# Optimization experiments

Hardware: AMD Instinct MI355X
Metric: run time of the kernel (lower is better)

Reference implementation:

```python
import jax, jax.numpy as jnp
import numpy as np

B, T, D, R, DFF = 4, 4096, 1024, 128, 4096
WINDOW = 1024
EPS = 1e-6


def rmsnorm(x, w):
    x32 = x.astype(jnp.float32)
    rms = jax.lax.rsqrt(jnp.mean(x32 * x32, axis=-1, keepdims=True) + EPS)
    return (x32 * rms).astype(x.dtype) * w


def rope(x, cos, sin):
    # x: (B, T, R); cos/sin: (T, R//2)
    d = x.shape[-1] // 2
    x1, x2 = x[..., :d], x[..., d:]
    return jnp.concatenate([x1 * cos + x2 * sin, -x1 * sin + x2 * cos], axis=-1)


def setup_inputs() -> dict:
    key = jax.random.key(0)
    ks = jax.random.split(key, 12)
    s = 0.02  # realistic weight scale
    return {
        "x": jax.random.normal(ks[0], (B, T, D), jnp.float32),
        "Uq": jax.random.normal(ks[1], (R, D), jnp.float32) * s,
        "Uk": jax.random.normal(ks[2], (R, D), jnp.float32) * s,
        "Uv": jax.random.normal(ks[3], (R, D), jnp.float32) * s,
        "cos": jnp.cos(jnp.outer(jnp.arange(T, dtype=jnp.float32),
                                 1.0 / (10000.0 ** (jnp.arange(R // 2, dtype=jnp.float32) / (R // 2))))),
        "sin": jnp.sin(jnp.outer(jnp.arange(T, dtype=jnp.float32),
                                 1.0 / (10000.0 ** (jnp.arange(R // 2, dtype=jnp.float32) / (R // 2))))),
        "ln1_w": jnp.ones((D,), jnp.float32),
        "ln2_w": jnp.ones((D,), jnp.float32),
        "Wo": jax.random.normal(ks[4], (D, R), jnp.float32) * s,
        "w1": jax.random.normal(ks[5], (DFF, D), jnp.float32) * s,
        "w3": jax.random.normal(ks[6], (DFF, D), jnp.float32) * s,
        "w2": jax.random.normal(ks[7], (D, DFF), jnp.float32) * s,
        "window_size": WINDOW,
    }


def reference(x, Uq, Uk, Uv, cos, sin, ln1_w, ln2_w, Wo, w1, w3, w2, window_size):
    Bx, Tx, _ = x.shape
    rank = Uq.shape[0]
    normed = rmsnorm(x, ln1_w)
    q = rope(normed @ Uq.T, cos, sin)  # (B, T, R)
    k = rope(normed @ Uk.T, cos, sin)
    v = normed @ Uv.T
    # windowed causal single-head SDPA
    scale = 1.0 / jnp.sqrt(jnp.float32(rank))
    scores = jnp.einsum("btr,bsr->bts", q, k) * scale  # (B, T, T)
    row = jnp.arange(Tx)[:, None]
    col = jnp.arange(Tx)[None, :]
    mask = (col <= row) & ((row - col) <= window_size)
    scores = jnp.where(mask, scores, jnp.float32(-jnp.inf))
    attn = jax.nn.softmax(scores, axis=-1)
    y = jnp.einsum("bts,bsr->btr", attn, v)  # (B, T, R)
    x = x + y @ Wo.T
    h = rmsnorm(x, ln2_w)
    ffn = ((h @ w1.T) * jax.nn.silu(h @ w3.T)) @ w2.T
    return x + ffn
```

## Files before the change

### kernel.cpp

```cpp
#include <hip/hip_runtime.h>
#include <hip/hip_bf16.h>
#include <stdint.h>

#define BT   16384
#define TT   4096
#define NB   4
#define DD   1024
#define RR   128
#define DFFC 4096

typedef __bf16 bf16_8 __attribute__((ext_vector_type(8)));
typedef float  f32x4  __attribute__((ext_vector_type(4)));

__device__ __forceinline__ void async16(const void* g, void* l) {
  __builtin_amdgcn_global_load_lds((__attribute__((address_space(1))) void*)(g),
                                   (__attribute__((address_space(3))) void*)(l),
                                   16, 0, 0);
}

__global__ __launch_bounds__(256) void cvt_k(const float* __restrict__ src,
                                             __hip_bfloat16* __restrict__ dst, int n4) {
  const int i = blockIdx.x * 256 + threadIdx.x;
  if (i >= n4) return;
  const float4 v = ((const float4*)src)[i];
  __hip_bfloat16* o = dst + (size_t)i * 4;
  o[0] = __float2bfloat16(v.x);
  o[1] = __float2bfloat16(v.y);
  o[2] = __float2bfloat16(v.z);
  o[3] = __float2bfloat16(v.w);
}

__global__ __launch_bounds__(256) void rmsnorm_k(const float* __restrict__ x,
                                                 const float* __restrict__ wgt,
                                                 __hip_bfloat16* __restrict__ out) {
  const int row = blockIdx.x;
  const int t = threadIdx.x;
  const float4 v = ((const float4*)(x + (size_t)row * DD))[t];
  float ss = v.x*v.x + v.y*v.y + v.z*v.z + v.w*v.w;
  #pragma unroll
  for (int m = 1; m < 64; m <<= 1) ss += __shfl_xor(ss, m, 64);
  __shared__ float red[4];
  if ((t & 63) == 0) red[t >> 6] = ss;
  __syncthreads();
  ss = red[0] + red[1] + red[2] + red[3];
  const float rms = rsqrtf(ss * (1.0f / DD) + 1e-6f);
  const float4 wv = ((const float4*)wgt)[t];
  __hip_bfloat16* o = out + (size_t)row * DD + t * 4;
  o[0] = __float2bfloat16(v.x * rms * wv.x);
  o[1] = __float2bfloat16(v.y * rms * wv.y);
  o[2] = __float2bfloat16(v.z * rms * wv.z);
  o[3] = __float2bfloat16(v.w * rms * wv.w);
}

__global__ __launch_bounds__(256) void rope_k(const __hip_bfloat16* __restrict__ qkv,
                                              const float* __restrict__ cosb,
                                              const float* __restrict__ sinb,
                                              __hip_bfloat16* __restrict__ qr,
                                              __hip_bfloat16* __restrict__ kr) {
  const int idx = blockIdx.x * 256 + threadIdx.x;
  const int row = idx >> 6;
  const int i = idx & 63;
  const int tpos = row & (TT - 1);
  const float c = cosb[tpos * 64 + i];
  const float s = sinb[tpos * 64 + i];
  const size_t base = (size_t)row * 384;
  const float q1 = __bfloat162float(qkv[base + i]);
  const float q2 = __bfloat162float(qkv[base + 64 + i]);
  const float k1 = __bfloat162float(qkv[base + 128 + i]);
  const float k2 = __bfloat162float(qkv[base + 192 + i]);
  const size_t ob = (size_t)row * 128;
  qr[ob + i]      = __float2bfloat16( q1 * c + q2 * s);
  qr[ob + 64 + i] = __float2bfloat16(-q1 * s + q2 * c);
  kr[ob + i]      = __float2bfloat16( k1 * c + k2 * s);
  kr[ob + 64 + i] = __float2bfloat16(-k1 * s + k2 * c);
}

__global__ __launch_bounds__(256) void vtrans_k(const __hip_bfloat16* __restrict__ qkv,
                                                __hip_bfloat16* __restrict__ Vt) {
  const int b = blockIdx.y, t0 = blockIdx.x * 64, t = threadIdx.x;
  #pragma unroll
  for (int i = 0; i < 4; ++i) {
    const int flat8 = i * 256 + t;
    const int row = flat8 >> 4;
    const int d8 = (flat8 & 15) * 8;
    const bf16_8 v = *(const bf16_8*)&qkv[((size_t)(b * TT + t0 + row)) * 384 + 256 + d8];
    #pragma unroll
    for (int j = 0; j < 8; ++j)
      ((__bf16*)Vt)[((size_t)(b * 128 + d8 + j)) * TT + t0 + row] = v[j];
  }
}

enum { EPI_BF16 = 0, EPI_RESID = 1, EPI_GATE = 2 };

template <int EPI>
__global__ __launch_bounds__(256) void gemm_bt(
    const __hip_bfloat16* __restrict__ A,
    const __hip_bfloat16* __restrict__ Bw,
    const float* __restrict__ resid,
    const __hip_bfloat16* __restrict__ gate,
    __hip_bfloat16* __restrict__ outb,
    float* __restrict__ outf,
    int N, int K) {
  __shared__ __hip_bfloat16 As[128 * 64];
  __shared__ __hip_bfloat16 Bs[128 * 64];
  const int t = threadIdx.x;
  const int w = t >> 6, lane = t & 63;
  const int wm = w >> 1, wn = w & 1;
  const int quad = lane >> 4, l16 = lane & 15;
  const int m0 = blockIdx.y * 128, n0 = blockIdx.x * 128;

  const __hip_bfloat16* Ab = A + (size_t)m0 * K;
  const __hip_bfloat16* Bb = Bw + (size_t)n0 * K;

  const int rloc = w * 8 + (lane >> 3);
  const int c0 = (((lane & 7) ^ ((lane >> 3) & 7)) << 3);
  const int swz = (l16 & 7);

  f32x4 acc[4][4] = {};

  for (int k0 = 0; k0 < K; k0 += 64) {
    #pragma unroll
    for (int j = 0; j < 4; ++j) {
      async16(Ab + (size_t)(j * 32 + rloc) * K + k0 + c0, &As[j * 2048 + w * 512]);
      async16(Bb + (size_t)(j * 32 + rloc) * K + k0 + c0, &Bs[j * 2048 + w * 512]);
    }
    __syncthreads();
    #pragma unroll
    for (int kc = 0; kc < 2; ++kc) {
      bf16_8 af[4], bfr[4];
      #pragma unroll
      for (int i = 0; i < 4; ++i) {
        const int pos = (((kc * 4 + quad) ^ swz) << 3);
        af[i]  = *(const bf16_8*)&As[(wm * 64 + i * 16 + l16) * 64 + pos];
        bfr[i] = *(const bf16_8*)&Bs[(wn * 64 + i * 16 + l16) * 64 + pos];
      }
      #pragma unroll
      for (int mt = 0; mt < 4; ++mt) {
        #pragma unroll
        for (int nt = 0; nt < 4; ++nt)
          acc[mt][nt] = __builtin_amdgcn_mfma_f32_16x16x32_bf16(af[mt], bfr[nt], acc[mt][nt], 0, 0, 0);
      }
    }
    __syncthreads();
  }

  #pragma unroll
  for (int mt = 0; mt < 4; ++mt) {
    #pragma unroll
    for (int nt = 0; nt < 4; ++nt) {
      #pragma unroll
      for (int r = 0; r < 4; ++r) {
        const int row = m0 + wm * 64 + mt * 16 + quad * 4 + r;
        const int col = n0 + wn * 64 + nt * 16 + l16;
        const size_t idx = (size_t)row * N + col;
        const float v = acc[mt][nt][r];
        if (EPI == EPI_BF16) {
          outb[idx] = __float2bfloat16(v);
        } else if (EPI == EPI_RESID) {
          outf[idx] = resid[idx] + v;
        } else {
          const float sv = v / (1.0f + __expf(-v));
          outb[idx] = __float2bfloat16(__bfloat162float(gate[idx]) * sv);
        }
      }
    }
  }
}

#define G256_BAR()  asm volatile("s_barrier" ::: "memory")
#define G256_VMW(N) asm volatile("s_waitcnt vmcnt(" #N ")" ::: "memory")

#define G256_DSA(mh_) \
  { _Pragma("unroll") for (int mt = 0; mt < 4; ++mt) { \
      const int rb_ = (rbA + (mh_) * 64 + mt * 16) * 64; \
      a[mt][0] = *(const bf16_8*)&Ac[rb_ + p0]; \
      a[mt][1] = *(const bf16_8*)&Ac[rb_ + p1]; } }

#define G256_DSB(nh_) \
  { _Pragma("unroll") for (int nt = 0; nt < 2; ++nt) { \
      const int rb_ = (rbB + (nh_) * 32 + nt * 16) * 64; \
      b[nt][0] = *(const bf16_8*)&Bc[rb_ + p0]; \
      b[nt][1] = *(const bf16_8*)&Bc[rb_ + p1]; } }

#define G256_MMA(mh_, nh_) \
  { __builtin_amdgcn_s_setprio(1); \
    _Pragma("unroll") for (int kk = 0; kk < 2; ++kk) \
      _Pragma("unroll") for (int mt = 0; mt < 4; ++mt) \
        _Pragma("unroll") for (int nt = 0; nt < 2; ++nt) \
          acc[(mh_) * 4 + mt][(nh_) * 2 + nt] = __builtin_amdgcn_mfma_f32_16x16x32_bf16( \
              a[mt][kk], b[nt][kk], acc[(mh_) * 4 + mt][(nh_) * 2 + nt], 0, 0, 0); \
    __builtin_amdgcn_s_setprio(0); }

#define G256_TILE(CUR, kt_) { \
    const __hip_bfloat16* Ac = As[CUR]; \
    const __hip_bfloat16* Bc = Bs[CUR]; \
    const int nb_ = (CUR) ^ 1; \
    const bool pf = ((kt_) + 1) < NT; \
    const int kn = ((kt_) + 1) << 6; \
     \
    G256_DSA(0); G256_DSB(0); \
    if (pf) { stageA(0, nb_, kn); stageB(0, nb_, kn); } \
    G256_BAR(); G256_MMA(0, 0); \
    if (pf) { G256_VMW(6); } else { G256_VMW(2); } \
    G256_BAR(); \
     \
    G256_DSB(1); \
    if (pf) { stageB(1, nb_, kn); } \
    G256_BAR(); G256_MMA(0, 1); \
    if (pf) { G256_VMW(6); } else { G256_VMW(0); } \
    G256_BAR(); \
     \
    G256_DSA(1); \
    if (pf) { stageA(1, nb_, kn); } \
    G256_BAR(); G256_MMA(1, 1); \
    G256_BAR(); \
     \
    G256_DSB(0); \
    G256_BAR(); G256_MMA(1, 0); \
    if (pf) { G256_VMW(4); } \
    G256_BAR(); \
  }

template <int EPI>
__global__ __launch_bounds__(512, 2) void gemm256(
    const __hip_bfloat16* __restrict__ A,
    const __hip_bfloat16* __restrict__ Bw,
    const float* __restrict__ resid,
    const __hip_bfloat16* __restrict__ gate,
    __hip_bfloat16* __restrict__ outb,
    float* __restrict__ outf,
    int N, int K) {
  __shared__ __hip_bfloat16 As[2][256 * 64];
  __shared__ __hip_bfloat16 Bs[2][256 * 64];
  const int t = threadIdx.x;
  const int w = t >> 6, lane = t & 63;
  const int wm = w >> 2, wn = w & 3;
  const int quad = lane >> 4, l16 = lane & 15;

  const int gx = gridDim.x;
  const int nwg = gx * gridDim.y;
  int lin = blockIdx.y * gx + blockIdx.x;
  lin = (lin & 7) * (nwg >> 3) + (lin >> 3);
  const int m0 = (lin / gx) * 256;
  const int n0 = (lin % gx) * 256;

  const __hip_bfloat16* Ab = A + (size_t)m0 * K;
  const __hip_bfloat16* Bb = Bw + (size_t)n0 * K;

  const int rl = lane >> 3;
  const int c0 = (((lane & 7) ^ rl) << 3);

  auto stageA = [&](int h, int buf, int k0) {
    const int r0 = h * 64 + (w << 3);
    async16(Ab + (size_t)(r0 + rl) * K + k0 + c0, &As[buf][r0 * 64]);
    const int r1 = r0 + 128;
    async16(Ab + (size_t)(r1 + rl) * K + k0 + c0, &As[buf][r1 * 64]);
  };
  auto stageB = [&](int h, int buf, int k0) {
    const int s0 = (w >> 2) * 64 + h * 32 + (w & 3) * 8;
    async16(Bb + (size_t)(s0 + rl) * K + k0 + c0, &Bs[buf][s0 * 64]);
    const int s1 = s0 + 128;
    async16(Bb + (size_t)(s1 + rl) * K + k0 + c0, &Bs[buf][s1 * 64]);
  };

  const int rbA = wm * 128 + l16;
  const int rbB = wn * 64 + l16;
  const int p0 = ((quad ^ (l16 & 7)) << 3);
  const int p1 = (((4 + quad) ^ (l16 & 7)) << 3);

  f32x4 acc[8][4] = {};
  bf16_8 a[4][2], b[2][2];
  const int NT = K >> 6;

  stageA(0, 0, 0); stageB(0, 0, 0); stageB(1, 0, 0); stageA(1, 0, 0);
  G256_VMW(4); G256_BAR();

  for (int kt = 0; kt < NT; kt += 2) {
    G256_TILE(0, kt);
    G256_TILE(1, kt + 1);
  }

  #pragma unroll
  for (int mf = 0; mf < 8; ++mf) {
    #pragma unroll
    for (int nf = 0; nf < 4; ++nf) {
      #pragma unroll
      for (int r = 0; r < 4; ++r) {
        const int row = m0 + wm * 128 + mf * 16 + quad * 4 + r;
        const int col = n0 + wn * 64 + nf * 16 + l16;
        const size_t idx = (size_t)row * N + col;
        const float v = acc[mf][nf][r];
        if (EPI == EPI_BF16) {
          outb[idx] = __float2bfloat16(v);
        } else if (EPI == EPI_RESID) {
          outf[idx] = resid[idx] + v;
        } else {
          const float sv = v / (1.0f + __expf(-v));
          outb[idx] = __float2bfloat16(__bfloat162float(gate[idx]) * sv);
        }
      }
    }
  }
}

__global__ __launch_bounds__(256) void attn_k(const __hip_bfloat16* __restrict__ qr,
                                              const __hip_bfloat16* __restrict__ kr,
                                              const __hip_bfloat16* __restrict__ Vt,
                                              __hip_bfloat16* __restrict__ y,
                                              const int* __restrict__ winp) {
  __shared__ __hip_bfloat16 Ksm[64 * 128];
  __shared__ __hip_bfloat16 Vsm[128 * 64];
  __shared__ __hip_bfloat16 Psm[4 * 16 * 72];
  const int t = threadIdx.x, w = t >> 6, lane = t & 63;
  const int quad = lane >> 4, l16 = lane & 15;
  const int b = blockIdx.y, t0 = blockIdx.x * 64;
  const int tw0 = t0 + w * 16;
  const int win = *winp;
  int kb_lo = t0 - win;
  if (kb_lo < 0) kb_lo = 0;
  kb_lo &= ~63;

  bf16_8 qf[4];
  const __hip_bfloat16* qb = qr + ((size_t)(b * TT + tw0 + l16)) * 128 + quad * 8;
  #pragma unroll
  for (int kk = 0; kk < 4; ++kk) qf[kk] = *(const bf16_8*)(qb + kk * 32);

  f32x4 o[8] = {};
  float mrow[4] = {-1e30f, -1e30f, -1e30f, -1e30f};
  float lrow[4] = {0.f, 0.f, 0.f, 0.f};
  const float scale = 0.08838834764831845f;

  const int krow_loc = (w * 4) + (lane >> 4);
  const int kc = ((lane & 15) ^ (krow_loc & 15)) << 3;
  const int vloc = lane >> 3;
  const int vc = ((lane & 7) ^ vloc) << 3;

  for (int kb0 = kb_lo; kb0 <= t0; kb0 += 64) {
    const __hip_bfloat16* kbp = kr + ((size_t)(b * TT + kb0)) * 128;
    #pragma unroll
    for (int i = 0; i < 4; ++i) {
      const int krow = i * 16 + krow_loc;
      async16(kbp + (size_t)krow * 128 + kc, &Ksm[i * 2048 + w * 512]);
    }
    #pragma unroll
    for (int i = 0; i < 4; ++i) {
      const int d0 = (i * 4 + w) * 8;
      const int dr = d0 + vloc;
      async16(Vt + ((size_t)(b * 128 + dr)) * TT + kb0 + vc, &Vsm[d0 * 64]);
    }
    __syncthreads();

    f32x4 s[4] = {};
    #pragma unroll
    for (int kk = 0; kk < 4; ++kk) {
      #pragma unroll
      for (int nt = 0; nt < 4; ++nt) {
        const int cc = ((kk * 4 + quad) ^ l16) << 3;
        const bf16_8 bfrag = *(const bf16_8*)&Ksm[(nt * 16 + l16) * 128 + cc];
        s[nt] = __builtin_amdgcn_mfma_f32_16x16x32_bf16(qf[kk], bfrag, s[nt], 0, 0, 0);
      }
    }

    float mb[4] = {-1e30f, -1e30f, -1e30f, -1e30f};
    #pragma unroll
    for (int nt = 0; nt < 4; ++nt) {
      #pragma unroll
      for (int r = 0; r < 4; ++r) {
        const int tq = tw0 + quad * 4 + r;
        const int scol = kb0 + nt * 16 + l16;
        float v = s[nt][r] * scale;
        const bool ok = (scol <= tq) && (tq - scol <= win);
        v = ok ? v : -1e30f;
        s[nt][r] = v;
        mb[r] = fmaxf(mb[r], v);
      }
    }

    #pragma unroll
    for (int r = 0; r < 4; ++r) {
      float m = mb[r];
      m = fmaxf(m, __shfl_xor(m, 1, 16));
      m = fmaxf(m, __shfl_xor(m, 2, 16));
      m = fmaxf(m, __shfl_xor(m, 4, 16));
      m = fmaxf(m, __shfl_xor(m, 8, 16));
      const float mn = fmaxf(mrow[r], m);
      const float alpha = __expf(mrow[r] - mn);
      mrow[r] = mn;
      float rs = 0.f;
      #pragma unroll
      for (int nt = 0; nt < 4; ++nt) {
        const float pv = __expf(s[nt][r] - mn);
        s[nt][r] = pv;
        rs += pv;
      }
      rs += __shfl_xor(rs, 1, 16);
      rs += __shfl_xor(rs, 2, 16);
      rs += __shfl_xor(rs, 4, 16);
      rs += __shfl_xor(rs, 8, 16);
      lrow[r] = lrow[r] * alpha + rs;
      #pragma unroll
      for (int n2 = 0; n2 < 8; ++n2) o[n2][r] *= alpha;
    }

    __hip_bfloat16* pw = &Psm[w * 1152];
    #pragma unroll
    for (int nt = 0; nt < 4; ++nt) {
      #pragma unroll
      for (int r = 0; r < 4; ++r)
        pw[(quad * 4 + r) * 72 + nt * 16 + l16] = __float2bfloat16(s[nt][r]);
    }
    asm volatile("s_waitcnt lgkmcnt(0)" ::: "memory");

    #pragma unroll
    for (int kk2 = 0; kk2 < 2; ++kk2) {
      const bf16_8 pa = *(const bf16_8*)&Psm[w * 1152 + l16 * 72 + kk2 * 32 + quad * 8];
      #pragma unroll
      for (int n2 = 0; n2 < 8; ++n2) {
        const int cc = ((kk2 * 4 + quad) ^ (l16 & 7)) << 3;
        const bf16_8 vb = *(const bf16_8*)&Vsm[(n2 * 16 + l16) * 64 + cc];
        o[n2] = __builtin_amdgcn_mfma_f32_16x16x32_bf16(pa, vb, o[n2], 0, 0, 0);
      }
    }
    __syncthreads();
  }

  #pragma unroll
  for (int n2 = 0; n2 < 8; ++n2) {
    #pragma unroll
    for (int r = 0; r < 4; ++r) {
      const int row = b * TT + tw0 + quad * 4 + r;
      const int col = n2 * 16 + l16;
      y[(size_t)row * 128 + col] = __float2bfloat16(o[n2][r] / lrow[r]);
    }
  }
}

extern "C" void kernel_launch(void* const* d_in, const int* in_sizes, int n_in,
                              void* d_out, int out_size, void* d_ws, size_t ws_size,
                              hipStream_t stream) {
  const float* x    = (const float*)d_in[0];
  const float* Uq   = (const float*)d_in[1];
  const float* Uk   = (const float*)d_in[2];
  const float* Uv   = (const float*)d_in[3];
  const float* cosb = (const float*)d_in[4];
  const float* sinb = (const float*)d_in[5];
  const float* ln1  = (const float*)d_in[6];
  const float* ln2  = (const float*)d_in[7];
  const float* Wo   = (const float*)d_in[8];
  const float* w1   = (const float*)d_in[9];
  const float* w3   = (const float*)d_in[10];
  const float* w2   = (const float*)d_in[11];
  const int*   winp = (const int*)d_in[12];
  float* out = (float*)d_out;

  uint8_t* p = (uint8_t*)d_ws;
  auto take = [&](size_t bytes) {
    uint8_t* q = p;
    p += (bytes + 255) & ~(size_t)255;
    return q;
  };

  __hip_bfloat16* h1     = (__hip_bfloat16*)take((size_t)BT * DFFC * 2);
  __hip_bfloat16* gb     = h1;
  __hip_bfloat16* normed = (__hip_bfloat16*)take((size_t)BT * DD * 2);
  __hip_bfloat16* hb     = normed;
  __hip_bfloat16* qkv    = (__hip_bfloat16*)take((size_t)BT * 384 * 2);
  __hip_bfloat16* yb     = qkv;
  __hip_bfloat16* qr_    = (__hip_bfloat16*)take((size_t)BT * RR * 2);
  __hip_bfloat16* kr_    = (__hip_bfloat16*)take((size_t)BT * RR * 2);
  __hip_bfloat16* Vt     = (__hip_bfloat16*)take((size_t)BT * RR * 2);
  __hip_bfloat16* Ucat   = (__hip_bfloat16*)take((size_t)384 * DD * 2);
  __hip_bfloat16* Wob    = (__hip_bfloat16*)take((size_t)DD * RR * 2);
  __hip_bfloat16* W1b    = (__hip_bfloat16*)take((size_t)DFFC * DD * 2);
  __hip_bfloat16* W3b    = (__hip_bfloat16*)take((size_t)DFFC * DD * 2);
  __hip_bfloat16* W2b    = (__hip_bfloat16*)take((size_t)DD * DFFC * 2);
  float* x_mid = out;

  cvt_k<<<128, 256, 0, stream>>>(Uq, Ucat, RR * DD / 4);
  cvt_k<<<128, 256, 0, stream>>>(Uk, Ucat + (size_t)RR * DD, RR * DD / 4);
  cvt_k<<<128, 256, 0, stream>>>(Uv, Ucat + (size_t)2 * RR * DD, RR * DD / 4);
  cvt_k<<<128, 256, 0, stream>>>(Wo, Wob, DD * RR / 4);
  cvt_k<<<4096, 256, 0, stream>>>(w1, W1b, DFFC * DD / 4);
  cvt_k<<<4096, 256, 0, stream>>>(w3, W3b, DFFC * DD / 4);
  cvt_k<<<4096, 256, 0, stream>>>(w2, W2b, DD * DFFC / 4);

  rmsnorm_k<<<BT, 256, 0, stream>>>(x, ln1, normed);

  gemm_bt<EPI_BF16><<<dim3(3, 128), 256, 0, stream>>>(normed, Ucat, nullptr, nullptr,
                                                      qkv, nullptr, 384, DD);

  rope_k<<<BT * 64 / 256, 256, 0, stream>>>(qkv, cosb, sinb, qr_, kr_);
  vtrans_k<<<dim3(TT / 64, NB), 256, 0, stream>>>(qkv, Vt);

  attn_k<<<dim3(TT / 64, NB), 256, 0, stream>>>(qr_, kr_, Vt, yb, winp);

  gemm_bt<EPI_RESID><<<dim3(8, 128), 256, 0, stream>>>(yb, Wob, x, nullptr,
                                                       nullptr, x_mid, DD, RR);

  rmsnorm_k<<<BT, 256, 0, stream>>>(x_mid, ln2, hb);

  gemm256<EPI_BF16><<<dim3(16, 64), 512, 0, stream>>>(hb, W1b, nullptr, nullptr,
                                                      h1, nullptr, DFFC, DD);
  gemm256<EPI_GATE><<<dim3(16, 64), 512, 0, stream>>>(hb, W3b, nullptr, h1,
                                                      gb, nullptr, DFFC, DD);
  gemm256<EPI_RESID><<<dim3(4, 64), 512, 0, stream>>>(gb, W2b, x_mid, nullptr,
                                                      nullptr, out, DD, DFFC);
}
```

Measured before the change: 777.6 us.

## Double-buffer GEMM fragment registers and prefetch next tile's fragments early

```diff
diff --git a/kernel.cpp b/kernel.cpp
--- a/kernel.cpp
+++ b/kernel.cpp
@@ -170,54 +170,55 @@
 #define G256_BAR()  asm volatile("s_barrier" ::: "memory")
 #define G256_VMW(N) asm volatile("s_waitcnt vmcnt(" #N ")" ::: "memory")
 
-#define G256_DSA(mh_) \
+#define G256_DSA_INTO(dst, mh_, SRC) \
   { _Pragma("unroll") for (int mt = 0; mt < 4; ++mt) { \
       const int rb_ = (rbA + (mh_) * 64 + mt * 16) * 64; \
-      a[mt][0] = *(const bf16_8*)&Ac[rb_ + p0]; \
-      a[mt][1] = *(const bf16_8*)&Ac[rb_ + p1]; } }
-
-#define G256_DSB(nh_) \
+      dst[mt][0] = *(const bf16_8*)&SRC[rb_ + p0]; \
+      dst[mt][1] = *(const bf16_8*)&SRC[rb_ + p1]; } }
+
+#define G256_DSB_INTO(dst, nh_, SRC) \
   { _Pragma("unroll") for (int nt = 0; nt < 2; ++nt) { \
       const int rb_ = (rbB + (nh_) * 32 + nt * 16) * 64; \
-      b[nt][0] = *(const bf16_8*)&Bc[rb_ + p0]; \
-      b[nt][1] = *(const bf16_8*)&Bc[rb_ + p1]; } }
-
-#define G256_MMA(mh_, nh_) \
+      dst[nt][0] = *(const bf16_8*)&SRC[rb_ + p0]; \
+      dst[nt][1] = *(const bf16_8*)&SRC[rb_ + p1]; } }
+
+#define G256_MMA(aset, bset, mh_, nh_) \
   { __builtin_amdgcn_s_setprio(1); \
     _Pragma("unroll") for (int kk = 0; kk < 2; ++kk) \
       _Pragma("unroll") for (int mt = 0; mt < 4; ++mt) \
         _Pragma("unroll") for (int nt = 0; nt < 2; ++nt) \
           acc[(mh_) * 4 + mt][(nh_) * 2 + nt] = __builtin_amdgcn_mfma_f32_16x16x32_bf16( \
-              a[mt][kk], b[nt][kk], acc[(mh_) * 4 + mt][(nh_) * 2 + nt], 0, 0, 0); \
+              aset[mt][kk], bset[nt][kk], acc[(mh_) * 4 + mt][(nh_) * 2 + nt], 0, 0, 0); \
     __builtin_amdgcn_s_setprio(0); }
 
 #define G256_TILE(CUR, kt_) { \
     const __hip_bfloat16* Ac = As[CUR]; \
     const __hip_bfloat16* Bc = Bs[CUR]; \
+    const __hip_bfloat16* An = As[(CUR) ^ 1]; \
+    const __hip_bfloat16* Bn = Bs[(CUR) ^ 1]; \
     const int nb_ = (CUR) ^ 1; \
     const bool pf = ((kt_) + 1) < NT; \
     const int kn = ((kt_) + 1) << 6; \
      \
-    G256_DSA(0); G256_DSB(0); \
+    G256_DSB_INTO(bQ, 1, Bc); \
     if (pf) { stageA(0, nb_, kn); stageB(0, nb_, kn); } \
-    G256_BAR(); G256_MMA(0, 0); \
-    if (pf) { G256_VMW(6); } else { G256_VMW(2); } \
+    G256_BAR(); G256_MMA(aP, bP, 0, 0); \
+    if (pf) { G256_VMW(4); } else { G256_VMW(0); } \
     G256_BAR(); \
      \
-    G256_DSB(1); \
+    G256_DSA_INTO(aQ, 1, Ac); \
     if (pf) { stageB(1, nb_, kn); } \
-    G256_BAR(); G256_MMA(0, 1); \
-    if (pf) { G256_VMW(6); } else { G256_VMW(0); } \
+    G256_BAR(); G256_MMA(aP, bQ, 0, 1); \
     G256_BAR(); \
      \
-    G256_DSA(1); \
     if (pf) { stageA(1, nb_, kn); } \
-    G256_BAR(); G256_MMA(1, 1); \
+    G256_BAR(); G256_MMA(aQ, bQ, 1, 1); \
+    if (pf) { G256_VMW(4); } \
     G256_BAR(); \
      \
-    G256_DSB(0); \
-    G256_BAR(); G256_MMA(1, 0); \
-    if (pf) { G256_VMW(4); } \
+    if (pf) { G256_DSA_INTO(aP, 0, An); } \
+    G256_BAR(); G256_MMA(aQ, bP, 1, 0); \
+    if (pf) { G256_DSB_INTO(bP, 0, Bn); G256_VMW(2); } \
     G256_BAR(); \
   }
 
@@ -269,11 +270,13 @@
   const int p1 = (((4 + quad) ^ (l16 & 7)) << 3);
 
   f32x4 acc[8][4] = {};
-  bf16_8 a[4][2], b[2][2];
+  bf16_8 aP[4][2], aQ[4][2], bP[2][2], bQ[2][2];
   const int NT = K >> 6;
 
   stageA(0, 0, 0); stageB(0, 0, 0); stageB(1, 0, 0); stageA(1, 0, 0);
   G256_VMW(4); G256_BAR();
+  G256_DSA_INTO(aP, 0, As[0]); G256_DSB_INTO(bP, 0, Bs[0]);
+  G256_VMW(2); G256_BAR();
 
   for (int kt = 0; kt < NT; kt += 2) {
     G256_TILE(0, kt);
```

After: 1.320 ms. 69.8% more time.
